# Optimization experiments

Measured on AMD Instinct MI355X. Metric: run time of the kernel, lower is better.

## Reference

```python
import jax, jax.numpy as jnp
import numpy as np

# Qwen3-Next GatedDeltaNet dims
H = 2048          # hidden_size
HK = 16           # linear_num_key_heads
HV = 32           # linear_num_value_heads
DK = 128          # linear_key_head_dim
DV = 128          # linear_value_head_dim
KDIM = HK * DK    # 2048
VDIM = HV * DV    # 4096
CONV_DIM = 2 * KDIM + VDIM  # 8192
KSIZE = 4         # linear_conv_kernel_dim
KV_RATIO = HV // HK
EPS = 1e-6        # rms_norm_eps
T = 1024


def setup_inputs() -> dict:
    key = jax.random.key(0)
    ks = jax.random.split(key, 8)
    s = lambda k, shape, sc=0.02: jax.random.normal(k, shape, jnp.float32) * sc
    return dict(
        hidden_states=jax.random.normal(ks[0], (1, T, H), jnp.float32),
        W_qkvz=s(ks[1], (H, 2 * KDIM + 2 * VDIM)),
        W_ba=s(ks[2], (H, 2 * HV)),
        conv_w=s(ks[3], (CONV_DIM, KSIZE), 0.2),   # depthwise, no bias
        dt_bias=jax.random.normal(ks[4], (HV,), jnp.float32) * 0.1,
        A_log=jnp.log(jax.random.uniform(ks[5], (HV,), jnp.float32, minval=1e-2, maxval=16.0)),
        norm_w=jnp.ones((DV,), jnp.float32),
        W_out=s(ks[6], (VDIM, H)),
    )


def _l2norm(x):
    # fla l2norm: x / sqrt(sum(x^2) + eps)
    return x * jax.lax.rsqrt(jnp.sum(x * x, axis=-1, keepdims=True) + 1e-6)


def reference(hidden_states, W_qkvz, W_ba, conv_w, dt_bias, A_log, norm_w, W_out):
    B, Tn, _ = hidden_states.shape
    qkvz = hidden_states @ W_qkvz                       # [B,T,2K+2V]
    ba = hidden_states @ W_ba                           # [B,T,2*HV]

    # fix_query_key_value_ordering: per k-head interleaved layout
    qkvz = qkvz.reshape(B, Tn, HK, 2 * DK + 2 * KV_RATIO * DV)
    q = qkvz[..., :DK]                                  # [B,T,HK,DK]
    k = qkvz[..., DK:2 * DK]
    v = qkvz[..., 2 * DK:2 * DK + KV_RATIO * DV].reshape(B, Tn, HV, DV)
    z = qkvz[..., 2 * DK + KV_RATIO * DV:].reshape(B, Tn, HV, DV)
    ba = ba.reshape(B, Tn, HK, 2 * KV_RATIO)
    b = ba[..., :KV_RATIO].reshape(B, Tn, HV)
    a = ba[..., KV_RATIO:].reshape(B, Tn, HV)

    # causal depthwise conv1d (no bias) + silu, single contiguous sequence
    mixed = jnp.concatenate([q.reshape(B, Tn, KDIM), k.reshape(B, Tn, KDIM),
                             v.reshape(B, Tn, VDIM)], axis=-1)   # [B,T,C]
    x = mixed.transpose(0, 2, 1)                                   # [B,C,T]
    x = jnp.pad(x, ((0, 0), (0, 0), (KSIZE - 1, 0)))
    y = jax.lax.conv_general_dilated(x, conv_w[:, None, :], (1,), 'VALID',
                                     feature_group_count=CONV_DIM)
    y = jax.nn.silu(y).transpose(0, 2, 1)                          # [B,T,C]
    q = y[..., :KDIM].reshape(B, Tn, HK, DK)
    k = y[..., KDIM:2 * KDIM].reshape(B, Tn, HK, DK)
    v = y[..., 2 * KDIM:].reshape(B, Tn, HV, DV)

    beta = jax.nn.sigmoid(b)                                       # [B,T,HV]
    g = -jnp.exp(A_log) * jax.nn.softplus(a + dt_bias)             # [B,T,HV] (log decay)

    # qk l2norm in kernel + fla default scale on q; GQA head repeat
    q = jnp.repeat(_l2norm(q), KV_RATIO, axis=2) * (DK ** -0.5)    # [B,T,HV,DK]
    k = jnp.repeat(_l2norm(k), KV_RATIO, axis=2)

    def scan_one(qs, ks, vs, gs, bs):
        def step(S, inp):
            qt, kt, vt, gt, bt = inp                    # per-head slices
            S = S * jnp.exp(gt)[:, None, None]          # gated decay, [HV,DK,DV]
            kv = jnp.einsum('hk,hkv->hv', kt, S)        # current memory readout
            delta = (vt - kv) * bt[:, None]             # delta rule with beta gate
            S = S + kt[:, :, None] * delta[:, None, :]
            o = jnp.einsum('hk,hkv->hv', qt, S)
            return S, o
        S0 = jnp.zeros((HV, DK, DV), qs.dtype)
        _, out = jax.lax.scan(step, S0, (qs, ks, vs, gs, bs))
        return out                                      # [T,HV,DV]

    core = jax.vmap(scan_one)(q, k, v, g, beta)         # [B,T,HV,DV]

    # gated RMSNorm per value head: x*silu(z) then rmsnorm, then weight
    gated = core * jax.nn.silu(z)
    gated = gated * jax.lax.rsqrt(jnp.mean(gated * gated, axis=-1, keepdims=True) + EPS)
    gated = gated * norm_w

    return gated.reshape(B, Tn, VDIM) @ W_out           # [B,T,H]
```

## Files before the change

### kernel.cpp

```cpp
#include <hip/hip_runtime.h>
#include <hip/hip_bf16.h>
#include <math.h>


#define T_LEN 1024
#define HK_N 16
#define HV_N 32
#define NQKVZ 12288
#define CHUNK 64
#define NCHUNK 16

typedef __bf16 bf16x8 __attribute__((ext_vector_type(8)));
typedef float f32x4 __attribute__((ext_vector_type(4)));

__device__ __forceinline__ ushort4 pack4(const f32x4 v) {
  ushort4 o;
  o.x = __bfloat16_as_ushort(__float2bfloat16(v[0]));
  o.y = __bfloat16_as_ushort(__float2bfloat16(v[1]));
  o.z = __bfloat16_as_ushort(__float2bfloat16(v[2]));
  o.w = __bfloat16_as_ushort(__float2bfloat16(v[3]));
  return o;
}

template <int BM, bool BF16OUT>
__global__ __launch_bounds__(256) void gemm_bf16(const __hip_bfloat16* __restrict__ A,
                                                 const __hip_bfloat16* __restrict__ B,
                                                 void* __restrict__ Cv,
                                                 int M, int N, int Klen, int ldk) {
  constexpr int AITS = BM / 32;
  constexpr int MF = BM / 32;
  __shared__ __align__(16) __hip_bfloat16 As[2][BM * 64];
  __shared__ __align__(16) __hip_bfloat16 Bs[2][128 * 64];
  const int tid = threadIdx.x;
  const int wid = tid >> 6, lane = tid & 63;
  const int wr = wid >> 1, wc = wid & 1;
  const int m0 = blockIdx.y * BM, n0 = blockIdx.x * 128;
  const size_t kbase = (size_t)blockIdx.z * Klen;
  const int lrow = lane & 15, lk = lane >> 4;
  const int rswz = (lrow & 7) * 8;
  f32x4 acc[MF][4] = {};
  const int nk = Klen >> 6;

#define GSTAGE(b_, k0_) do {                                                    \
    _Pragma("unroll") for (int it = 0; it < AITS; ++it) {                       \
      const int c_ = it * 256 + tid;                                            \
      const int row_ = c_ >> 3;                                                 \
      const int col8_ = ((c_ & 7) ^ (row_ & 7)) * 8;                            \
      __builtin_amdgcn_global_load_lds(                                         \
          (const __attribute__((address_space(1))) void*)                       \
              (A + (size_t)(m0 + row_) * ldk + kbase + (k0_) + col8_),          \
          (__attribute__((address_space(3))) void*)(&As[b_][it * 2048 + tid * 8]), 16, 0, 0); \
    }                                                                           \
    _Pragma("unroll") for (int it = 0; it < 4; ++it) {                          \
      const int c_ = it * 256 + tid;                                            \
      const int row_ = c_ >> 3;                                                 \
      const int col8_ = ((c_ & 7) ^ (row_ & 7)) * 8;                            \
      __builtin_amdgcn_global_load_lds(                                         \
          (const __attribute__((address_space(1))) void*)                       \
              (B + (size_t)(n0 + row_) * ldk + kbase + (k0_) + col8_),          \
          (__attribute__((address_space(3))) void*)(&Bs[b_][it * 2048 + tid * 8]), 16, 0, 0); \
    }                                                                           \
  } while (0)

  GSTAGE(0, 0);
  int buf = 0;
  for (int k = 0; k < nk; ++k) {
    if (k + 1 < nk) {
      GSTAGE(buf ^ 1, (k + 1) << 6);
      if constexpr (BM == 128) asm volatile("s_waitcnt vmcnt(8)" ::: "memory");
      else                     asm volatile("s_waitcnt vmcnt(6)" ::: "memory");
    } else {
      asm volatile("s_waitcnt vmcnt(0)" ::: "memory");
    }
    __builtin_amdgcn_s_barrier();
    __builtin_amdgcn_sched_barrier(0);
#pragma unroll
    for (int kk = 0; kk < 2; ++kk) {
      bf16x8 af[MF], bfv[4];
#pragma unroll
      for (int m = 0; m < MF; ++m)
        af[m] = *reinterpret_cast<const bf16x8*>(
            &As[buf][(wr * (BM / 2) + m * 16 + lrow) * 64 + ((kk * 32 + lk * 8) ^ rswz)]);
#pragma unroll
      for (int n = 0; n < 4; ++n)
        bfv[n] = *reinterpret_cast<const bf16x8*>(
            &Bs[buf][(wc * 64 + n * 16 + lrow) * 64 + ((kk * 32 + lk * 8) ^ rswz)]);
#pragma unroll
      for (int m = 0; m < MF; ++m)
#pragma unroll
        for (int n = 0; n < 4; ++n)
          acc[m][n] = __builtin_amdgcn_mfma_f32_16x16x32_bf16(af[m], bfv[n], acc[m][n], 0, 0, 0);
    }
    __builtin_amdgcn_sched_barrier(0);
    __builtin_amdgcn_s_barrier();
    buf ^= 1;
  }
#undef GSTAGE
  if constexpr (BF16OUT) {
    __hip_bfloat16* Cz = (__hip_bfloat16*)Cv + (size_t)blockIdx.z * M * N;
#pragma unroll
    for (int m = 0; m < MF; ++m)
#pragma unroll
      for (int n = 0; n < 4; ++n)
#pragma unroll
        for (int r = 0; r < 4; ++r)
          Cz[(size_t)(m0 + wr * (BM / 2) + m * 16 + lk * 4 + r) * N + n0 + wc * 64 + n * 16 + lrow] =
              __float2bfloat16(acc[m][n][r]);
  } else {
    float* Cz = (float*)Cv + (size_t)blockIdx.z * M * N;
#pragma unroll
    for (int m = 0; m < MF; ++m)
#pragma unroll
      for (int n = 0; n < 4; ++n)
#pragma unroll
        for (int r = 0; r < 4; ++r)
          Cz[(size_t)(m0 + wr * (BM / 2) + m * 16 + lk * 4 + r) * N + n0 + wc * 64 + n * 16 + lrow] =
              acc[m][n][r];
  }
}

__global__ void add4(const __hip_bfloat16* __restrict__ P, float* __restrict__ out, int n) {
  const int i = (blockIdx.x * 256 + threadIdx.x) * 4;
  if (i < n) {
    float s[4] = {0.f, 0.f, 0.f, 0.f};
#pragma unroll
    for (int z = 0; z < 4; ++z) {
      const ushort4 v = *reinterpret_cast<const ushort4*>(P + (size_t)z * n + i);
      s[0] += __bfloat162float(__ushort_as_bfloat16(v.x));
      s[1] += __bfloat162float(__ushort_as_bfloat16(v.y));
      s[2] += __bfloat162float(__ushort_as_bfloat16(v.z));
      s[3] += __bfloat162float(__ushort_as_bfloat16(v.w));
    }
    *reinterpret_cast<float4*>(out + i) = make_float4(s[0], s[1], s[2], s[3]);
  }
}

__global__ __launch_bounds__(256) void prep2(const float* __restrict__ X,
                                             __hip_bfloat16* __restrict__ Xb,
                                             const float* __restrict__ Wq,
                                             __hip_bfloat16* __restrict__ Wqt,
                                             const float* __restrict__ Wba,
                                             float* __restrict__ P) {
  __shared__ __align__(16) float smem[16 * 512];
  const int bid = blockIdx.x;
  const int tid = threadIdx.x;
  if (bid < 2048) {
    const int i = (bid * 256 + tid) * 4;
    const float4 v = *reinterpret_cast<const float4*>(X + i);
    ushort4 o;
    o.x = __bfloat16_as_ushort(__float2bfloat16(v.x));
    o.y = __bfloat16_as_ushort(__float2bfloat16(v.y));
    o.z = __bfloat16_as_ushort(__float2bfloat16(v.z));
    o.w = __bfloat16_as_ushort(__float2bfloat16(v.w));
    *reinterpret_cast<ushort4*>((void*)(Xb + i)) = o;
  } else if (bid < 8192) {
    float (*tl)[65] = reinterpret_cast<float (*)[65]>(smem);
    const int b = bid - 2048;
    const int n0 = (b % 192) * 64, k0 = (b / 192) * 64;
    const int N = NQKVZ, K = 2048;
    const int rc = tid & 15, rr = tid >> 4;
#pragma unroll
    for (int i = 0; i < 4; ++i) {
      const int k = rr + 16 * i;
      const float4 v = *reinterpret_cast<const float4*>(&Wq[(size_t)(k0 + k) * N + n0 + rc * 4]);
      tl[k][rc * 4 + 0] = v.x;
      tl[k][rc * 4 + 1] = v.y;
      tl[k][rc * 4 + 2] = v.z;
      tl[k][rc * 4 + 3] = v.w;
    }
    __syncthreads();
    const int wcx = tid & 7, wry = tid >> 3;
#pragma unroll
    for (int i = 0; i < 2; ++i) {
      const int n = wry + 32 * i;
      uint u[8];
#pragma unroll
      for (int j = 0; j < 8; ++j)
        u[j] = __bfloat16_as_ushort(__float2bfloat16(tl[wcx * 8 + j][n]));
      uint4 o;
      o.x = u[0] | (u[1] << 16);
      o.y = u[2] | (u[3] << 16);
      o.z = u[4] | (u[5] << 16);
      o.w = u[6] | (u[7] << 16);
      *reinterpret_cast<uint4*>((void*)&Wqt[(size_t)(n0 + n) * K + k0 + wcx * 8]) = o;
    }
  } else {
    float (*Xs)[512] = reinterpret_cast<float (*)[512]>(smem);
    const int b = bid - 8192;
    const int tt = b & 63, ks = b >> 6;
    const int c = tid & 63, r4 = tid >> 6;
    const float* xsrc = X + (size_t)(tt * 16) * 2048 + ks * 512;
#pragma unroll
    for (int u = 0; u < 8; ++u) {
      const int flat = (u * 256 + tid) * 4;
      const int r = flat >> 9, k = flat & 511;
      *reinterpret_cast<float4*>(&Xs[r][k]) =
          *reinterpret_cast<const float4*>(&xsrc[(size_t)r * 2048 + k]);
    }
    __syncthreads();
    float acc[4] = {};
    const float* wp = Wba + (size_t)(ks * 512) * 64 + c;
    for (int k = 0; k < 512; k += 8) {
      float w[8];
#pragma unroll
      for (int u = 0; u < 8; ++u) w[u] = wp[(size_t)(k + u) * 64];
#pragma unroll
      for (int u = 0; u < 8; ++u)
#pragma unroll
        for (int i = 0; i < 4; ++i)
          acc[i] = fmaf(Xs[r4 * 4 + i][k + u], w[u], acc[i]);
    }
    float* pp = P + ((size_t)ks * 1024 + tt * 16 + r4 * 4) * 64 + c;
#pragma unroll
    for (int i = 0; i < 4; ++i) pp[(size_t)i * 64] = acc[i];
  }
}

__global__ __launch_bounds__(256) void convs(const __hip_bfloat16* __restrict__ qkvz,
                                             const float* __restrict__ conv_w,
                                             float* __restrict__ QK,
                                             float* __restrict__ V,
                                             const float* __restrict__ P,
                                             const float* __restrict__ dt_bias,
                                             const float* __restrict__ A_log,
                                             float* __restrict__ gg,
                                             float* __restrict__ bet) {
  const int bid = blockIdx.x;
  const int tid = threadIdx.x;
  if (bid < 4096) {
    const int kh = bid & 15;
    const int t = (bid >> 4) * 4 + (tid >> 6);
    const int l = tid & 63;
    const int cols[4] = {kh * 768 + l, kh * 768 + l + 64,
                         kh * 768 + 128 + l, kh * 768 + 128 + l + 64};
    const int chs[4] = {kh * 128 + l, kh * 128 + l + 64,
                        2048 + kh * 128 + l, 2048 + kh * 128 + l + 64};
    float y[4];
#pragma unroll
    for (int j = 0; j < 4; ++j) {
      const float* wp = &conv_w[chs[j] * 4];
      float acc = 0.f;
#pragma unroll
      for (int s = 0; s < 4; ++s) {
        const int tt = t - 3 + s;
        if (tt >= 0)
          acc = fmaf(__bfloat162float(qkvz[(size_t)tt * NQKVZ + cols[j]]), wp[s], acc);
      }
      y[j] = acc / (1.f + expf(-acc));
    }
    float sq = y[0] * y[0] + y[1] * y[1];
    float sk = y[2] * y[2] + y[3] * y[3];
#pragma unroll
    for (int off = 32; off; off >>= 1) {
      sq += __shfl_xor(sq, off);
      sk += __shfl_xor(sk, off);
    }
    const float rq = rsqrtf(sq + 1e-6f) * 0.08838834764831845f;
    const float rk = rsqrtf(sk + 1e-6f);
    const size_t qb = (size_t)t * 4096 + kh * 128;
    QK[qb + l] = y[0] * rq;
    QK[qb + l + 64] = y[1] * rq;
    QK[qb + 2048 + l] = y[2] * rk;
    QK[qb + 2048 + l + 64] = y[3] * rk;
  } else if (bid < 4608) {
    const int b = bid - 4096;
    const int c2 = (b & 15) * 256 + tid;
    const int vh = c2 >> 7;
    const int col = (vh >> 1) * 768 + 256 + (vh & 1) * 128 + (c2 & 127);
    const int t0 = (b >> 4) * 32;
    const float4 w = *reinterpret_cast<const float4*>(&conv_w[(4096 + c2) * 4]);
    float x0, x1, x2;
    if (t0 == 0) {
      x0 = 0.f; x1 = 0.f; x2 = 0.f;
    } else {
      x0 = __bfloat162float(qkvz[(size_t)(t0 - 3) * NQKVZ + col]);
      x1 = __bfloat162float(qkvz[(size_t)(t0 - 2) * NQKVZ + col]);
      x2 = __bfloat162float(qkvz[(size_t)(t0 - 1) * NQKVZ + col]);
    }
#pragma unroll 4
    for (int tt = 0; tt < 32; ++tt) {
      const int t = t0 + tt;
      const float x3 = __bfloat162float(qkvz[(size_t)t * NQKVZ + col]);
      float acc = x0 * w.x;
      acc = fmaf(x1, w.y, acc);
      acc = fmaf(x2, w.z, acc);
      acc = fmaf(x3, w.w, acc);
      V[(size_t)t * 4096 + c2] = acc / (1.f + expf(-acc));
      x0 = x1; x1 = x2; x2 = x3;
    }
  } else {
    const int idx = (bid - 4608) * 256 + tid;
    const int t = idx >> 5, vh = idx & 31;
    const int cb = (vh >> 1) * 4 + (vh & 1);
    float b = 0.f, a = 0.f;
#pragma unroll
    for (int s = 0; s < 4; ++s) {
      b += P[((size_t)s * 1024 + t) * 64 + cb];
      a += P[((size_t)s * 1024 + t) * 64 + cb + 2];
    }
    const float x = a + dt_bias[vh];
    const float sp = (x > 20.f) ? x : log1pf(expf(x));
    gg[idx] = -expf(A_log[vh]) * sp;
    bet[idx] = 1.f / (1.f + expf(-b));
  }
}

__global__ __launch_bounds__(256, 2) void phase1(
    const float* __restrict__ QK, const float* __restrict__ V,
    const float* __restrict__ g, const float* __restrict__ bet,
    __hip_bfloat16* __restrict__ Ub, __hip_bfloat16* __restrict__ Wb,
    __hip_bfloat16* __restrict__ KTb, __hip_bfloat16* __restrict__ Qgb,
    __hip_bfloat16* __restrict__ Bb, float* __restrict__ gend) {
  const int vh = blockIdx.x, ch = blockIdx.y, kh = vh >> 1;
  const int tid = threadIdx.x;
  const int t0 = ch * CHUNK;
  __shared__ __align__(16) float Kl[64][132];
  __shared__ __align__(16) float Al[64][68];
  __shared__ float bs[64], gams[64], bets[64], lams[64];

  const int row = tid >> 2;
  const size_t hb = (size_t)ch * 32 + vh;
  {
    const int cc = (tid & 3) * 32;
    const float* src = &QK[(size_t)(t0 + row) * 4096 + 2048 + kh * 128 + cc];
#pragma unroll
    for (int u = 0; u < 32; u += 4)
      *reinterpret_cast<float4*>(&Kl[row][cc + u]) =
          *reinterpret_cast<const float4*>(src + u);
  }
  if (tid < 64) {
    float b = g[(size_t)(t0 + tid) * 32 + vh];
#pragma unroll
    for (int off = 1; off < 64; off <<= 1) {
      const float o = __shfl_up(b, off);
      if (tid >= off) b += o;
    }
    const float b63 = __shfl(b, 63);
    const float ga = expf(b);
    bs[tid] = b;
    gams[tid] = ga;
    lams[tid] = expf(b63 - b);
    bets[tid] = bet[(size_t)(t0 + tid) * 32 + vh];
    if (tid == 63) gend[ch * 32 + vh] = ga;
  }
  __syncthreads();
  {
    const int i = tid & 63;
    const float li = lams[i];
    __hip_bfloat16* kt = &KTb[hb * 128 * 64];
    const int dbase = (tid >> 6) * 32;
#pragma unroll
    for (int dd = 0; dd < 32; ++dd) {
      const int d = dbase + dd;
      kt[(size_t)d * 64 + (i ^ ((d & 7) << 3))] = __float2bfloat16(li * Kl[i][d]);
    }
  }
  {
    const int j0 = (tid & 3) * 16;
    const float* qrow = &QK[(size_t)(t0 + row) * 4096 + kh * 128];
    const float gai = gams[row];
    __hip_bfloat16* qg = &Qgb[(hb * 64 + row) * 128];
    float accA[16], accB[16];
#pragma unroll
    for (int jj = 0; jj < 16; ++jj) { accA[jj] = 0.f; accB[jj] = 0.f; }
    for (int d = 0; d < 128; d += 4) {
      const float4 qi = *reinterpret_cast<const float4*>(qrow + d);
      const float4 ki = *reinterpret_cast<const float4*>(&Kl[row][d]);
      if ((d >> 5) == (tid & 3)) {
        ushort4 qq;
        qq.x = __bfloat16_as_ushort(__float2bfloat16(gai * qi.x));
        qq.y = __bfloat16_as_ushort(__float2bfloat16(gai * qi.y));
        qq.z = __bfloat16_as_ushort(__float2bfloat16(gai * qi.z));
        qq.w = __bfloat16_as_ushort(__float2bfloat16(gai * qi.w));
        *reinterpret_cast<ushort4*>(&qg[d ^ ((row & 7) << 3)]) = qq;
      }
#pragma unroll
      for (int jj = 0; jj < 16; ++jj) {
        const float4 kj = *reinterpret_cast<const float4*>(&Kl[j0 + jj][d]);
        accA[jj] += ki.x * kj.x + ki.y * kj.y + ki.z * kj.z + ki.w * kj.w;
        accB[jj] += qi.x * kj.x + qi.y * kj.y + qi.z * kj.z + qi.w * kj.w;
      }
    }
    const float bi = bets[row], bvi = bs[row];
    __hip_bfloat16* Bout = &Bb[(hb * 64 + row) * 64];
#pragma unroll
    for (int jj = 0; jj < 16; ++jj) {
      const int j = j0 + jj;
      const float dec = expf(bvi - bs[j]);
      Al[row][j] = (j < row) ? bi * dec * accA[jj] : 0.f;
      Bout[j ^ ((row & 7) << 3)] =
          __float2bfloat16((j <= row) ? dec * accB[jj] : 0.f);
    }
  }
  __syncthreads();
  {
    const int cc = tid;
    float x[64];
    const bool isV = cc < 128;
    const float* src = isV ? &V[(size_t)t0 * 4096 + vh * 128 + cc]
                           : &QK[(size_t)t0 * 4096 + 2048 + kh * 128 + (cc - 128)];
#pragma unroll
    for (int i = 0; i < 64; ++i) {
      const float sc = isV ? bets[i] : bets[i] * gams[i];
      x[i] = sc * src[(size_t)i * 4096];
    }
#pragma unroll
    for (int i = 1; i < 64; ++i) {
      float s0 = 0.f, s1 = 0.f, s2 = 0.f, s3 = 0.f;
      int j = 0;
#pragma unroll
      for (; j + 4 <= i; j += 4) {
        const float4 a = *reinterpret_cast<const float4*>(&Al[i][j]);
        s0 = fmaf(a.x, x[j], s0);
        s1 = fmaf(a.y, x[j + 1], s1);
        s2 = fmaf(a.z, x[j + 2], s2);
        s3 = fmaf(a.w, x[j + 3], s3);
      }
#pragma unroll
      for (; j < i; ++j) s0 = fmaf(Al[i][j], x[j], s0);
      x[i] -= (s0 + s1) + (s2 + s3);
    }
    if (isV) {
      __hip_bfloat16* dst = &Ub[hb * 64 * 128 + cc];
#pragma unroll
      for (int i = 0; i < 64; ++i) dst[(size_t)i * 128] = __float2bfloat16(x[i]);
    } else {
      const int d = cc - 128;
      __hip_bfloat16* dst = &Wb[hb * 64 * 128];
#pragma unroll
      for (int i = 0; i < 64; ++i)
        dst[(size_t)i * 128 + (d ^ ((i & 7) << 3))] = __float2bfloat16(-x[i]);
    }
  }
}

__global__ __launch_bounds__(128) void phaseB(
    const __hip_bfloat16* __restrict__ Ug, const __hip_bfloat16* __restrict__ Wb,
    const __hip_bfloat16* __restrict__ KTb, const __hip_bfloat16* __restrict__ Qgb,
    const __hip_bfloat16* __restrict__ Bb, const float* __restrict__ gendg,
    float* __restrict__ Og) {
  const int vh = blockIdx.x, slice = blockIdx.y;
  const int tid = threadIdx.x, lane = tid & 63, w = tid >> 6;
  const int l15 = lane & 15, l4 = lane >> 4;
  const int cg = slice * 32 + w * 16;
  const int swz = (l15 & 7) << 3;

  __shared__ __hip_bfloat16 Wl[2][8192];
  __shared__ __hip_bfloat16 KTl[2][8192];
  __shared__ __hip_bfloat16 Qgl[2][8192];
  __shared__ __hip_bfloat16 Bl[2][4096];
  __shared__ __hip_bfloat16 Sop[2][2048];
  __shared__ __hip_bfloat16 dLs[2][1024];

  f32x4 accS[8] = {};
  for (int x = lane; x < 1024; x += 64) reinterpret_cast<uint*>(Sop[w])[x] = 0;

  float ubuf[4][4];
#define STAGE(b_, c_) do {                                                      \
    const size_t hb_ = ((size_t)(c_) * 32 + vh);                                \
    _Pragma("unroll") for (int it = 0; it < 8; ++it) {                          \
      __builtin_amdgcn_global_load_lds(                                         \
          (const __attribute__((address_space(1))) void*)(Wb + hb_ * 8192 + it * 1024 + tid * 8), \
          (__attribute__((address_space(3))) void*)(&Wl[b_][it * 1024 + tid * 8]), 16, 0, 0); \
      __builtin_amdgcn_global_load_lds(                                         \
          (const __attribute__((address_space(1))) void*)(KTb + hb_ * 8192 + it * 1024 + tid * 8), \
          (__attribute__((address_space(3))) void*)(&KTl[b_][it * 1024 + tid * 8]), 16, 0, 0); \
      __builtin_amdgcn_global_load_lds(                                         \
          (const __attribute__((address_space(1))) void*)(Qgb + hb_ * 8192 + it * 1024 + tid * 8), \
          (__attribute__((address_space(3))) void*)(&Qgl[b_][it * 1024 + tid * 8]), 16, 0, 0); \
      if (it < 4)                                                               \
        __builtin_amdgcn_global_load_lds(                                       \
            (const __attribute__((address_space(1))) void*)(Bb + hb_ * 4096 + it * 1024 + tid * 8), \
            (__attribute__((address_space(3))) void*)(&Bl[b_][it * 1024 + tid * 8]), 16, 0, 0); \
    }                                                                           \
  } while (0)
#define UPREF(c_) do {                                                          \
    const __hip_bfloat16* up_ = Ug + ((size_t)(c_) * 32 + vh) * 64 * 128 + cg + l15; \
    _Pragma("unroll") for (int m_ = 0; m_ < 4; ++m_)                            \
      _Pragma("unroll") for (int r_ = 0; r_ < 4; ++r_)                          \
        ubuf[m_][r_] = __bfloat162float(up_[(size_t)(m_ * 16 + l4 * 4 + r_) * 128]); \
  } while (0)

  STAGE(0, 0);
  UPREF(0);
  __syncthreads();
  int buf = 0;
  for (int ch = 0; ch < NCHUNK; ++ch) {
    if (ch + 1 < NCHUNK) STAGE(buf ^ 1, ch + 1);
    f32x4 acc_d[4];
#pragma unroll
    for (int m = 0; m < 4; ++m) {
      f32x4 t;
      t[0] = ubuf[m][0]; t[1] = ubuf[m][1]; t[2] = ubuf[m][2]; t[3] = ubuf[m][3];
      acc_d[m] = t;
    }
    if (ch + 1 < NCHUNK) UPREF(ch + 1);
#pragma unroll
    for (int t = 0; t < 4; ++t) {
      const bf16x8 bS = *reinterpret_cast<const bf16x8*>(
          &Sop[w][l15 * 128 + ((t * 32 + l4 * 8) ^ swz)]);
#pragma unroll
      for (int m = 0; m < 4; ++m) {
        const bf16x8 aW = *reinterpret_cast<const bf16x8*>(
            &Wl[buf][(m * 16 + l15) * 128 + ((t * 32 + l4 * 8) ^ swz)]);
        acc_d[m] = __builtin_amdgcn_mfma_f32_16x16x32_bf16(aW, bS, acc_d[m], 0, 0, 0);
      }
    }
#pragma unroll
    for (int m = 0; m < 4; ++m)
      *reinterpret_cast<ushort4*>(&dLs[w][l15 * 64 + ((m * 16 + l4 * 4) ^ swz)]) =
          pack4(acc_d[m]);
    f32x4 acc_o[4] = {};
#pragma unroll
    for (int t = 0; t < 4; ++t) {
      const bf16x8 bS = *reinterpret_cast<const bf16x8*>(
          &Sop[w][l15 * 128 + ((t * 32 + l4 * 8) ^ swz)]);
#pragma unroll
      for (int m = 0; m < 4; ++m) {
        const bf16x8 aQ = *reinterpret_cast<const bf16x8*>(
            &Qgl[buf][(m * 16 + l15) * 128 + ((t * 32 + l4 * 8) ^ swz)]);
        acc_o[m] = __builtin_amdgcn_mfma_f32_16x16x32_bf16(aQ, bS, acc_o[m], 0, 0, 0);
      }
    }
#pragma unroll
    for (int t2 = 0; t2 < 2; ++t2) {
      const bf16x8 bD = *reinterpret_cast<const bf16x8*>(
          &dLs[w][l15 * 64 + ((t2 * 32 + l4 * 8) ^ swz)]);
#pragma unroll
      for (int m = 0; m < 4; ++m) {
        const bf16x8 aB = *reinterpret_cast<const bf16x8*>(
            &Bl[buf][(m * 16 + l15) * 64 + ((t2 * 32 + l4 * 8) ^ swz)]);
        acc_o[m] = __builtin_amdgcn_mfma_f32_16x16x32_bf16(aB, bD, acc_o[m], 0, 0, 0);
      }
    }
    float* ob = Og + (size_t)(ch * 64) * 4096 + (size_t)vh * 128 + cg + l15;
#pragma unroll
    for (int m = 0; m < 4; ++m)
#pragma unroll
      for (int r = 0; r < 4; ++r)
        ob[(size_t)(m * 16 + l4 * 4 + r) * 4096] = acc_o[m][r];
    const float ge = gendg[ch * 32 + vh];
#pragma unroll
    for (int f = 0; f < 8; ++f) {
      accS[f][0] *= ge; accS[f][1] *= ge; accS[f][2] *= ge; accS[f][3] *= ge;
    }
#pragma unroll
    for (int t2 = 0; t2 < 2; ++t2) {
      const bf16x8 bD = *reinterpret_cast<const bf16x8*>(
          &dLs[w][l15 * 64 + ((t2 * 32 + l4 * 8) ^ swz)]);
#pragma unroll
      for (int f = 0; f < 8; ++f) {
        const bf16x8 aK = *reinterpret_cast<const bf16x8*>(
            &KTl[buf][(f * 16 + l15) * 64 + ((t2 * 32 + l4 * 8) ^ swz)]);
        accS[f] = __builtin_amdgcn_mfma_f32_16x16x32_bf16(aK, bD, accS[f], 0, 0, 0);
      }
    }
#pragma unroll
    for (int f = 0; f < 8; ++f)
      *reinterpret_cast<ushort4*>(&Sop[w][l15 * 128 + ((f * 16 + l4 * 4) ^ swz)]) =
          pack4(accS[f]);
    __syncthreads();
    buf ^= 1;
  }
#undef STAGE
#undef UPREF
}

__global__ __launch_bounds__(256) void gfuse(const float* __restrict__ O,
                                             const __hip_bfloat16* __restrict__ qkvz,
                                             const float* __restrict__ norm_w,
                                             __hip_bfloat16* __restrict__ G,
                                             const float* __restrict__ Wo,
                                             __hip_bfloat16* __restrict__ Wot) {
  __shared__ float tl[64][65];
  const int bid = blockIdx.x;
  const int tid = threadIdx.x;
  if (bid < 8192) {
    const int vh = (bid & 7) * 4 + (tid >> 6);
    const int t = bid >> 3, l = tid & 63;
    const size_t ob = (size_t)t * 4096 + vh * 128;
    const size_t zb = (size_t)t * NQKVZ + (vh >> 1) * 768 + 512 + (vh & 1) * 128;
    const float o0 = O[ob + l], o1 = O[ob + l + 64];
    const float z0 = __bfloat162float(qkvz[zb + l]);
    const float z1 = __bfloat162float(qkvz[zb + l + 64]);
    const float g0 = o0 * z0 / (1.f + expf(-z0));
    const float g1 = o1 * z1 / (1.f + expf(-z1));
    float ss = g0 * g0 + g1 * g1;
#pragma unroll
    for (int off = 32; off; off >>= 1) ss += __shfl_xor(ss, off);
    const float rr = rsqrtf(ss * (1.f / 128.f) + 1e-6f);
    G[ob + l] = __float2bfloat16(g0 * rr * norm_w[l]);
    G[ob + l + 64] = __float2bfloat16(g1 * rr * norm_w[l + 64]);
    return;
  }
  const int b = bid - 8192;
  const int n0 = (b & 31) * 64, k0 = (b >> 5) * 64;
  const int N = 2048, K = 4096;
  const int rc = tid & 15, rr2 = tid >> 4;
#pragma unroll
  for (int i = 0; i < 4; ++i) {
    const int k = rr2 + 16 * i;
    const float4 v = *reinterpret_cast<const float4*>(&Wo[(size_t)(k0 + k) * N + n0 + rc * 4]);
    tl[k][rc * 4 + 0] = v.x;
    tl[k][rc * 4 + 1] = v.y;
    tl[k][rc * 4 + 2] = v.z;
    tl[k][rc * 4 + 3] = v.w;
  }
  __syncthreads();
  const int wcx = tid & 7, wry = tid >> 3;
#pragma unroll
  for (int i = 0; i < 2; ++i) {
    const int n = wry + 32 * i;
    uint u[8];
#pragma unroll
    for (int j = 0; j < 8; ++j)
      u[j] = __bfloat16_as_ushort(__float2bfloat16(tl[wcx * 8 + j][n]));
    uint4 o;
    o.x = u[0] | (u[1] << 16);
    o.y = u[2] | (u[3] << 16);
    o.z = u[4] | (u[5] << 16);
    o.w = u[6] | (u[7] << 16);
    *reinterpret_cast<uint4*>((void*)&Wot[(size_t)(n0 + n) * K + k0 + wcx * 8]) = o;
  }
}

extern "C" void kernel_launch(void* const* d_in, const int* in_sizes, int n_in,
                              void* d_out, int out_size, void* d_ws, size_t ws_size,
                              hipStream_t stream) {
  const float* X = (const float*)d_in[0];
  const float* W_qkvz = (const float*)d_in[1];
  const float* W_ba = (const float*)d_in[2];
  const float* conv_w = (const float*)d_in[3];
  const float* dt_bias = (const float*)d_in[4];
  const float* A_log = (const float*)d_in[5];
  const float* norm_w = (const float*)d_in[6];
  const float* W_out = (const float*)d_in[7];
  float* out = (float*)d_out;

  float* ws = (float*)d_ws;
  float* qkvz = ws;
  float* P = qkvz + (size_t)T_LEN * NQKVZ;
  float* QK = P + 262144;
  float* V = QK + (size_t)T_LEN * 4096;
  float* U_f = V + (size_t)T_LEN * 4096;
  float* Wb_f = U_f + (size_t)NCHUNK * 32 * 64 * 128;
  float* KT_f = Wb_f + 2097152;
  float* Qg_f = KT_f + 2097152;
  float* Bb_f = Qg_f + 2097152;
  float* gg = Bb_f + 1048576;
  float* bet = gg + 32768;
  float* gend = bet + 32768;

  __hip_bfloat16* qkvzb = (__hip_bfloat16*)qkvz;
  __hip_bfloat16* Ub = (__hip_bfloat16*)U_f;
  __hip_bfloat16* Wb = (__hip_bfloat16*)Wb_f;
  __hip_bfloat16* KTb = (__hip_bfloat16*)KT_f;
  __hip_bfloat16* Qgb = (__hip_bfloat16*)Qg_f;
  __hip_bfloat16* Bb = (__hip_bfloat16*)Bb_f;
  __hip_bfloat16* Wqkvz_t = (__hip_bfloat16*)V;
  __hip_bfloat16* Xb = (__hip_bfloat16*)Qg_f;
  __hip_bfloat16* Gb = (__hip_bfloat16*)Bb_f;
  __hip_bfloat16* Wout_t = (__hip_bfloat16*)qkvz;
  float* O = V;
  __hip_bfloat16* Pout = (__hip_bfloat16*)U_f;

  prep2<<<dim3(2048 + 6144 + 256), 256, 0, stream>>>(X, Xb, W_qkvz, Wqkvz_t, W_ba, P);
  gemm_bf16<128, true><<<dim3(NQKVZ / 128, T_LEN / 128, 1), 256, 0, stream>>>(
      Xb, Wqkvz_t, qkvzb, T_LEN, NQKVZ, 2048, 2048);
  convs<<<dim3(4096 + 512 + 128), 256, 0, stream>>>(qkvzb, conv_w, QK, V, P,
                                                    dt_bias, A_log, gg, bet);
  phase1<<<dim3(HV_N, NCHUNK), 256, 0, stream>>>(QK, V, gg, bet, Ub, Wb, KTb, Qgb, Bb, gend);
  phaseB<<<dim3(HV_N, 4), 128, 0, stream>>>(Ub, Wb, KTb, Qgb, Bb, gend, O);
  gfuse<<<dim3(8192 + 2048), 256, 0, stream>>>(O, qkvzb, norm_w, Gb, W_out, Wout_t);
  gemm_bf16<128, true><<<dim3(2048 / 128, T_LEN / 128, 4), 256, 0, stream>>>(
      Gb, Wout_t, Pout, T_LEN, 2048, 1024, 4096);
  add4<<<dim3(T_LEN * 2048 / 4 / 256), 256, 0, stream>>>(Pout, out, T_LEN * 2048);
}
```

Measured before the change: 286.4 us.

## Use bf16 MFMA for intra-chunk K·Kᵀ and Q·Kᵀ in phase1

The chunk's K and Q tiles are now staged in shared memory as swizzled bf16 instead of fp32. The per-thread scalar FMA loops that computed the 64x64 K·Kᵀ and Q·Kᵀ products are replaced with 16x16x32 bf16 MFMA instructions, one 16-row strip per wave. This cuts the fp32 FFMA work and halves the shared-memory footprint of the K tile. In exchange, K and Q are rounded to bf16 before the products and before the decayed K writes, which adds precision loss to the A matrix feeding the triangular solve.

```diff
diff --git a/kernel.cpp b/kernel.cpp
--- a/kernel.cpp
+++ b/kernel.cpp
@@ -314,7 +314,8 @@
   const int vh = blockIdx.x, ch = blockIdx.y, kh = vh >> 1;
   const int tid = threadIdx.x;
   const int t0 = ch * CHUNK;
-  __shared__ __align__(16) float Kl[64][132];
+  __shared__ __align__(16) __hip_bfloat16 KbS[64][128];
+  __shared__ __align__(16) __hip_bfloat16 QbS[64][128];
   __shared__ __align__(16) float Al[64][68];
   __shared__ float bs[64], gams[64], bets[64], lams[64];
 
@@ -322,11 +323,26 @@
   const size_t hb = (size_t)ch * 32 + vh;
   {
     const int cc = (tid & 3) * 32;
-    const float* src = &QK[(size_t)(t0 + row) * 4096 + 2048 + kh * 128 + cc];
-#pragma unroll
-    for (int u = 0; u < 32; u += 4)
-      *reinterpret_cast<float4*>(&Kl[row][cc + u]) =
-          *reinterpret_cast<const float4*>(src + u);
+    const float* ksrc = &QK[(size_t)(t0 + row) * 4096 + 2048 + kh * 128 + cc];
+    const float* qsrc = &QK[(size_t)(t0 + row) * 4096 + kh * 128 + cc];
+#pragma unroll
+    for (int u = 0; u < 32; u += 4) {
+      const float4 kv = *reinterpret_cast<const float4*>(ksrc + u);
+      const float4 qv = *reinterpret_cast<const float4*>(qsrc + u);
+      const int d0 = cc + u;
+      const int sidx = (d0 & 7) | ((((d0 >> 3) ^ (row & 7)) & 15) << 3);
+      ushort4 kk4, qq4;
+      kk4.x = __bfloat16_as_ushort(__float2bfloat16(kv.x));
+      kk4.y = __bfloat16_as_ushort(__float2bfloat16(kv.y));
+      kk4.z = __bfloat16_as_ushort(__float2bfloat16(kv.z));
+      kk4.w = __bfloat16_as_ushort(__float2bfloat16(kv.w));
+      qq4.x = __bfloat16_as_ushort(__float2bfloat16(qv.x));
+      qq4.y = __bfloat16_as_ushort(__float2bfloat16(qv.y));
+      qq4.z = __bfloat16_as_ushort(__float2bfloat16(qv.z));
+      qq4.w = __bfloat16_as_ushort(__float2bfloat16(qv.w));
+      *reinterpret_cast<ushort4*>(&KbS[row][sidx]) = kk4;
+      *reinterpret_cast<ushort4*>(&QbS[row][sidx]) = qq4;
+    }
   }
   if (tid < 64) {
     float b = g[(size_t)(t0 + tid) * 32 + vh];
@@ -352,44 +368,57 @@
 #pragma unroll
     for (int dd = 0; dd < 32; ++dd) {
       const int d = dbase + dd;
-      kt[(size_t)d * 64 + (i ^ ((d & 7) << 3))] = __float2bfloat16(li * Kl[i][d]);
+      const int sidx = (d & 7) | ((((d >> 3) ^ (i & 7)) & 15) << 3);
+      kt[(size_t)d * 64 + (i ^ ((d & 7) << 3))] =
+          __float2bfloat16(li * __bfloat162float(KbS[i][sidx]));
     }
   }
   {
-    const int j0 = (tid & 3) * 16;
-    const float* qrow = &QK[(size_t)(t0 + row) * 4096 + kh * 128];
     const float gai = gams[row];
     __hip_bfloat16* qg = &Qgb[(hb * 64 + row) * 128];
-    float accA[16], accB[16];
-#pragma unroll
-    for (int jj = 0; jj < 16; ++jj) { accA[jj] = 0.f; accB[jj] = 0.f; }
-    for (int d = 0; d < 128; d += 4) {
-      const float4 qi = *reinterpret_cast<const float4*>(qrow + d);
-      const float4 ki = *reinterpret_cast<const float4*>(&Kl[row][d]);
-      if ((d >> 5) == (tid & 3)) {
-        ushort4 qq;
-        qq.x = __bfloat16_as_ushort(__float2bfloat16(gai * qi.x));
-        qq.y = __bfloat16_as_ushort(__float2bfloat16(gai * qi.y));
-        qq.z = __bfloat16_as_ushort(__float2bfloat16(gai * qi.z));
-        qq.w = __bfloat16_as_ushort(__float2bfloat16(gai * qi.w));
-        *reinterpret_cast<ushort4*>(&qg[d ^ ((row & 7) << 3)]) = qq;
+    const int cc = (tid & 3) * 32;
+#pragma unroll
+    for (int u = 0; u < 32; u += 4) {
+      const int d0 = cc + u;
+      const int sidx = (d0 & 7) | ((((d0 >> 3) ^ (row & 7)) & 15) << 3);
+      ushort4 qq;
+      qq.x = __bfloat16_as_ushort(__float2bfloat16(gai * __bfloat162float(QbS[row][sidx + 0])));
+      qq.y = __bfloat16_as_ushort(__float2bfloat16(gai * __bfloat162float(QbS[row][sidx + 1])));
+      qq.z = __bfloat16_as_ushort(__float2bfloat16(gai * __bfloat162float(QbS[row][sidx + 2])));
+      qq.w = __bfloat16_as_ushort(__float2bfloat16(gai * __bfloat162float(QbS[row][sidx + 3])));
+      *reinterpret_cast<ushort4*>(&qg[d0 ^ ((row & 7) << 3)]) = qq;
+    }
+  }
+  {
+    const int w = tid >> 6, lane = tid & 63;
+    const int lrow = lane & 15, lk = lane >> 4;
+    bf16x8 af[4], qf[4];
+#pragma unroll
+    for (int kk = 0; kk < 4; ++kk) {
+      const int c = ((kk * 4 + lk) ^ (lrow & 7)) * 8;
+      af[kk] = *reinterpret_cast<const bf16x8*>(&KbS[w * 16 + lrow][c]);
+      qf[kk] = *reinterpret_cast<const bf16x8*>(&QbS[w * 16 + lrow][c]);
+    }
+#pragma unroll
+    for (int n = 0; n < 4; ++n) {
+      f32x4 aA = {}, aB = {};
+#pragma unroll
+      for (int kk = 0; kk < 4; ++kk) {
+        const bf16x8 bf = *reinterpret_cast<const bf16x8*>(
+            &KbS[n * 16 + lrow][((kk * 4 + lk) ^ (lrow & 7)) * 8]);
+        aA = __builtin_amdgcn_mfma_f32_16x16x32_bf16(af[kk], bf, aA, 0, 0, 0);
+        aB = __builtin_amdgcn_mfma_f32_16x16x32_bf16(qf[kk], bf, aB, 0, 0, 0);
       }
-#pragma unroll
-      for (int jj = 0; jj < 16; ++jj) {
-        const float4 kj = *reinterpret_cast<const float4*>(&Kl[j0 + jj][d]);
-        accA[jj] += ki.x * kj.x + ki.y * kj.y + ki.z * kj.z + ki.w * kj.w;
-        accB[jj] += qi.x * kj.x + qi.y * kj.y + qi.z * kj.z + qi.w * kj.w;
+      __hip_bfloat16* Bout = &Bb[hb * 64 * 64];
+#pragma unroll
+      for (int r = 0; r < 4; ++r) {
+        const int i = w * 16 + lk * 4 + r;
+        const int j = n * 16 + lrow;
+        const float dec = expf(bs[i] - bs[j]);
+        Al[i][j] = (j < i) ? bets[i] * dec * aA[r] : 0.f;
+        Bout[(size_t)i * 64 + (j ^ ((i & 7) << 3))] =
+            __float2bfloat16((j <= i) ? dec * aB[r] : 0.f);
       }
-    }
-    const float bi = bets[row], bvi = bs[row];
-    __hip_bfloat16* Bout = &Bb[(hb * 64 + row) * 64];
-#pragma unroll
-    for (int jj = 0; jj < 16; ++jj) {
-      const int j = j0 + jj;
-      const float dec = expf(bvi - bs[j]);
-      Al[row][j] = (j < row) ? bi * dec * accA[jj] : 0.f;
-      Bout[j ^ ((row & 7) << 3)] =
-          __float2bfloat16((j <= row) ? dec * accB[jj] : 0.f);
     }
   }
   __syncthreads();
```

Result: faster. 265.0 us (-7.5%).
